# Performance work log

Measured on AMD Instinct MI355X. Metric: run time of the kernel, lower is better.

Reference implementation:

```python
import jax, jax.numpy as jnp
import numpy as np

DIM = 128      # channels C
HEADS = 4
HD = DIM // HEADS  # head_dim = 32
N = 128        # window tokens = 2*8*8
BW = 2048      # B_ = batch * num_windows
NP = 256       # sp_mask partitions
NW = 256       # shift-mask windows
TABLE = 675    # (2*2-1)*(2*8-1)*(2*8-1)
SCALE = HD ** -0.5


def setup_inputs() -> dict:
    key = jax.random.key(0)
    ks = jax.random.split(key, 8)
    x = jax.random.normal(ks[0], (BW, N, DIM), jnp.float32)
    rpi = jax.random.randint(ks[1], (N, N), 0, TABLE, dtype=jnp.int32)
    mask = jax.random.normal(ks[2], (NW, N, N), jnp.float32)
    sp_mask = jax.random.normal(ks[3], (NP, N, N), jnp.float32)
    w_qkv = jax.random.normal(ks[4], (3 * DIM, DIM), jnp.float32) * 0.02
    b_qkv = jnp.zeros((3 * DIM,), jnp.float32)
    bias_table = jax.random.normal(ks[5], (TABLE, HEADS), jnp.float32) * 0.02
    w_proj = jax.random.normal(ks[6], (DIM, DIM), jnp.float32) * 0.02
    b_proj = jnp.zeros((DIM,), jnp.float32)
    return {"x": x, "rpi": rpi, "mask": mask, "sp_mask": sp_mask,
            "w_qkv": w_qkv, "b_qkv": b_qkv, "bias_table": bias_table,
            "w_proj": w_proj, "b_proj": b_proj}


def reference(x, rpi, mask, sp_mask, w_qkv, b_qkv, bias_table, w_proj, b_proj):
    B_, Nn, C = x.shape
    # qkv projection -> (B_, N, 3, H, hd)
    qkv = (x @ w_qkv.T + b_qkv).reshape(B_, Nn, 3, HEADS, HD)
    q = qkv[:, :, 0].transpose(0, 2, 1, 3) * SCALE  # (B_, H, N, hd)
    k = qkv[:, :, 1].transpose(0, 2, 1, 3)
    v = qkv[:, :, 2].transpose(0, 2, 1, 3)
    attn = jnp.einsum('bhnd,bhmd->bhnm', q, k)  # (B_, H, N, N)
    # gathered relative position bias: (N, N, H) -> (H, N, N)
    rpb = bias_table[rpi].transpose(2, 0, 1)
    attn = attn + rpb[None]
    # additive sparse mask, broadcast over B_//nP groups and heads
    attn = (attn.reshape(B_ // NP, NP, HEADS, Nn, Nn)
            + sp_mask[None, :, None]).reshape(B_, HEADS, Nn, Nn)
    # additive shift mask, broadcast over B_//nW groups and heads
    attn = (attn.reshape(B_ // NW, NW, HEADS, Nn, Nn)
            + mask[None, :, None]).reshape(B_, HEADS, Nn, Nn)
    attn = jax.nn.softmax(attn, axis=-1)
    out = jnp.einsum('bhnm,bhmd->bnhd', attn, v).reshape(B_, Nn, C)
    return out @ w_proj.T + b_proj
```

## Files before the change

### kernel.cpp

```cpp
#include <hip/hip_runtime.h>

typedef short v8s __attribute__((ext_vector_type(8)));
typedef float v4f __attribute__((ext_vector_type(4)));

#define MFMA16(a, b, c) __builtin_amdgcn_mfma_f32_16x16x32_bf16(a, b, c, 0, 0, 0)

__device__ __forceinline__ unsigned short f2b(float f) {
  union { float f; unsigned int i; } v;
  v.f = f;
  unsigned int x = v.i;
  return (unsigned short)((x + 0x7fffu + ((x >> 16) & 1u)) >> 16);
}
__device__ __forceinline__ unsigned int cvtpk(float lo, float hi) {
  unsigned int r;
  asm("v_cvt_pk_bf16_f32 %0, %1, %2" : "=v"(r) : "v"(lo), "v"(hi));
  return r;
}

#define SCALE 0.17677669529663687f
#define LOG2E 1.4426950408889634f
#define QSCALE (SCALE * LOG2E)

#define WS_RPB 16777216
#define WS_WQH 17039360
#define WS_WPH 17137664

__global__ __launch_bounds__(256)
void conv_w(const float* __restrict__ wq, const float* __restrict__ wp,
            unsigned short* __restrict__ wqh, unsigned short* __restrict__ wph) {
  int i = blockIdx.x * 256 + threadIdx.x;
  if (i < 384 * 128) wqh[i] = f2b(wq[i]);
  else wph[i - 384 * 128] = f2b(wp[i - 384 * 128]);
}

__global__ __launch_bounds__(256)
void build_bias(const float* __restrict__ mask, const float* __restrict__ sp,
                const int* __restrict__ rpi, const float* __restrict__ btab,
                float* __restrict__ msum, float* __restrict__ rpb) {
  const int wgrp = blockIdx.x, tid = threadIdx.x;
  const float* mk = mask + (size_t)wgrp * 16384;
  const float* sk = sp + (size_t)wgrp * 16384;
  float* ot = msum + (size_t)wgrp * 16384;
  for (int it = 0; it < 16; ++it) {
    int i = (tid + 256 * it) * 4;
    float4 a = *(const float4*)(mk + i);
    float4 b = *(const float4*)(sk + i);
    float4 s;
    s.x = (a.x + b.x) * LOG2E; s.y = (a.y + b.y) * LOG2E;
    s.z = (a.z + b.z) * LOG2E; s.w = (a.w + b.w) * LOG2E;
    *(float4*)(ot + i) = s;
  }
  int e = wgrp * 256 + tid;
  int hh = e >> 14, r = e & 16383;
  rpb[e] = btab[rpi[r] * 4 + hh] * LOG2E;
}

__global__ __launch_bounds__(1024, 4)
void attn_fused(const float* __restrict__ xg,
                const unsigned short* __restrict__ wqh,
                const float* __restrict__ bq,
                const float* __restrict__ msum,
                const float* __restrict__ rpb,
                const unsigned short* __restrict__ wph,
                const float* __restrict__ bpj,
                float* __restrict__ out) {
  __shared__ alignas(16) unsigned char smem[110592];
  unsigned short* xs = (unsigned short*)smem;
  unsigned short* os = (unsigned short*)smem;

  const int tid = threadIdx.x;
  const int wid = tid >> 6;
  const int s = wid & 3;
  const int h = wid >> 2;
  const int lane = tid & 63;
  const int qd = lane >> 4;
  const int t16 = lane & 15;

  const int idx = blockIdx.x;
  const int wgrp = idx >> 3;
  const int b = (idx & 7) * 256 + wgrp;

  unsigned short* kss = (unsigned short*)(smem + 34816 + h * 10240);
  unsigned short* vs  = (unsigned short*)(smem + 75776 + h * 8704);

  {
    const float* src = xg + (size_t)b * 16384;
    for (int it = 0; it < 2; ++it) {
      int gl = tid + 1024 * it;
      int row = gl >> 4, g = gl & 15;
      const float4* s4 = (const float4*)(src + row * 128 + g * 8);
      float4 a = s4[0], c = s4[1];
      union { int4 v; unsigned int d[4]; } pk;
      pk.d[0] = cvtpk(a.x, a.y); pk.d[1] = cvtpk(a.z, a.w);
      pk.d[2] = cvtpk(c.x, c.y); pk.d[3] = cvtpk(c.z, c.w);
      *(int4*)(xs + row * 128 + ((g ^ (row & 15)) << 3)) = pk.v;
    }
  }
  __syncthreads();

  v8s bx[2][4];
  for (int nt = 0; nt < 2; ++nt)
    for (int ks = 0; ks < 4; ++ks) {
      int n = 32 * s + nt * 16 + t16;
      int g = ks * 4 + qd;
      bx[nt][ks] = *(const v8s*)(xs + n * 128 + ((g ^ (n & 15)) << 3));
    }

  v4f accqk[4][2];
  for (int jt = 0; jt < 4; ++jt)
    for (int nt = 0; nt < 2; ++nt) accqk[jt][nt] = v4f{0.f, 0.f, 0.f, 0.f};
  for (int jt = 0; jt < 4; ++jt) {
    int wbase = (jt < 2) ? (h * 32 + jt * 16) : (128 + h * 32 + (jt - 2) * 16);
    for (int ks = 0; ks < 4; ++ks) {
      v8s a = *(const v8s*)(wqh + (wbase + t16) * 128 + ks * 32 + 8 * qd);
      for (int nt = 0; nt < 2; ++nt)
        accqk[jt][nt] = MFMA16(a, bx[nt][ks], accqk[jt][nt]);
    }
  }
  v4f accv[2][2];
  for (int rt = 0; rt < 2; ++rt)
    for (int ct = 0; ct < 2; ++ct) accv[rt][ct] = v4f{0.f, 0.f, 0.f, 0.f};
  for (int ct = 0; ct < 2; ++ct)
    for (int ks = 0; ks < 4; ++ks) {
      v8s bw = *(const v8s*)(wqh + (256 + h * 32 + ct * 16 + t16) * 128 + ks * 32 + 8 * qd);
      for (int rt = 0; rt < 2; ++rt)
        accv[rt][ct] = MFMA16(bx[rt][ks], bw, accv[rt][ct]);
    }

  for (int jt = 2; jt < 4; ++jt)
    for (int nt = 0; nt < 2; ++nt) {
      int n = 32 * s + nt * 16 + t16;
      int bb = 128 + h * 32 + (jt - 2) * 16 + 4 * qd;
      uint2 pk;
      pk.x = cvtpk(accqk[jt][nt][0] + bq[bb + 0], accqk[jt][nt][1] + bq[bb + 1]);
      pk.y = cvtpk(accqk[jt][nt][2] + bq[bb + 2], accqk[jt][nt][3] + bq[bb + 3]);
      *(uint2*)(kss + n * 40 + (jt - 2) * 16 + 4 * qd) = pk;
    }
  for (int ct = 0; ct < 2; ++ct) {
    int d = ct * 16 + t16;
    float bv = bq[256 + h * 32 + d];
    for (int rt = 0; rt < 2; ++rt) {
      uint2 pk;
      pk.x = cvtpk(accv[rt][ct][0] + bv, accv[rt][ct][1] + bv);
      pk.y = cvtpk(accv[rt][ct][2] + bv, accv[rt][ct][3] + bv);
      *(uint2*)(vs + d * 136 + 32 * s + rt * 16 + 4 * qd) = pk;
    }
  }

  unsigned int qpk[2][2][2];
  for (int jt = 0; jt < 2; ++jt)
    for (int nt = 0; nt < 2; ++nt) {
      int bb = h * 32 + jt * 16 + 4 * qd;
      float v0 = (accqk[jt][nt][0] + bq[bb + 0]) * QSCALE;
      float v1 = (accqk[jt][nt][1] + bq[bb + 1]) * QSCALE;
      float v2 = (accqk[jt][nt][2] + bq[bb + 2]) * QSCALE;
      float v3 = (accqk[jt][nt][3] + bq[bb + 3]) * QSCALE;
      qpk[jt][nt][0] = cvtpk(v0, v1);
      qpk[jt][nt][1] = cvtpk(v2, v3);
    }
  const int srcA = ((qd & 1) << 5) + t16;
  const bool hiq = qd >= 2;
  v8s aq[2];
  for (int rt = 0; rt < 2; ++rt) {
    union { v8s v; unsigned int d[4]; } u;
    unsigned int a0 = __shfl((int)qpk[0][rt][0], srcA, 64);
    unsigned int b0 = __shfl((int)qpk[1][rt][0], srcA, 64);
    unsigned int a1 = __shfl((int)qpk[0][rt][1], srcA, 64);
    unsigned int b1 = __shfl((int)qpk[1][rt][1], srcA, 64);
    unsigned int a2 = __shfl((int)qpk[0][rt][0], srcA + 16, 64);
    unsigned int b2 = __shfl((int)qpk[1][rt][0], srcA + 16, 64);
    unsigned int a3 = __shfl((int)qpk[0][rt][1], srcA + 16, 64);
    unsigned int b3 = __shfl((int)qpk[1][rt][1], srcA + 16, 64);
    u.d[0] = hiq ? b0 : a0;
    u.d[1] = hiq ? b1 : a1;
    u.d[2] = hiq ? b2 : a2;
    u.d[3] = hiq ? b3 : a3;
    aq[rt] = u.v;
  }
  __syncthreads();

  v4f sa[2][8];
  const v4f zero4 = {0.f, 0.f, 0.f, 0.f};
  for (int ct = 0; ct < 8; ++ct) {
    v8s bk = *(const v8s*)(kss + (ct * 16 + t16) * 40 + 8 * qd);
    for (int nt = 0; nt < 2; ++nt)
      sa[nt][ct] = MFMA16(bk, aq[nt], zero4);
  }
  {
    const float* mt = msum + (size_t)wgrp * 16384;
    const float* rb = rpb + (size_t)h * 16384;
    for (int nt = 0; nt < 2; ++nt) {
      int n = 32 * s + nt * 16 + t16;
      const float* pm = mt + n * 128;
      const float* pr = rb + n * 128;
      for (int ct = 0; ct < 8; ++ct) {
        float4 b1 = *(const float4*)(pm + ct * 16 + 4 * qd);
        float4 b2 = *(const float4*)(pr + ct * 16 + 4 * qd);
        sa[nt][ct][0] += b1.x + b2.x;
        sa[nt][ct][1] += b1.y + b2.y;
        sa[nt][ct][2] += b1.z + b2.z;
        sa[nt][ct][3] += b1.w + b2.w;
      }
    }
  }
  float pinv[2];
  for (int nt = 0; nt < 2; ++nt) {
    float m0 = sa[nt][0][0];
    for (int ct = 0; ct < 8; ++ct)
      for (int r = 0; r < 4; ++r) m0 = fmaxf(m0, sa[nt][ct][r]);
    m0 = fmaxf(m0, __shfl_xor(m0, 16));
    m0 = fmaxf(m0, __shfl_xor(m0, 32));
    for (int ct = 0; ct < 8; ++ct)
      for (int r = 0; r < 4; ++r)
        sa[nt][ct][r] = exp2f(sa[nt][ct][r] - m0);
    float s0 = 0.f;
    for (int ct = 0; ct < 8; ++ct)
      for (int r = 0; r < 4; ++r) s0 += sa[nt][ct][r];
    s0 += __shfl_xor(s0, 16);
    s0 += __shfl_xor(s0, 32);
    pinv[nt] = 1.0f / s0;
  }

  v8s av[2][4];
  for (int rt = 0; rt < 2; ++rt)
    for (int ks = 0; ks < 4; ++ks)
      av[rt][ks] = *(const v8s*)(vs + (rt * 16 + t16) * 136 + ks * 32 + 8 * qd);

  const int srcP0 = ((qd & 1) << 5) + t16;
  const bool hip2 = qd >= 2;
  for (int nt = 0; nt < 2; ++nt) {
    unsigned int pkd[8][2];
    for (int ct = 0; ct < 8; ++ct) {
      pkd[ct][0] = cvtpk(sa[nt][ct][0], sa[nt][ct][1]);
      pkd[ct][1] = cvtpk(sa[nt][ct][2], sa[nt][ct][3]);
    }
    v8s bp[4];
    for (int ks = 0; ks < 4; ++ks) {
      union { v8s v; unsigned int d[4]; } u;
      unsigned int a0 = __shfl((int)pkd[2 * ks][0], srcP0, 64);
      unsigned int b0 = __shfl((int)pkd[2 * ks + 1][0], srcP0, 64);
      unsigned int a1 = __shfl((int)pkd[2 * ks][1], srcP0, 64);
      unsigned int b1 = __shfl((int)pkd[2 * ks + 1][1], srcP0, 64);
      unsigned int a2 = __shfl((int)pkd[2 * ks][0], srcP0 + 16, 64);
      unsigned int b2 = __shfl((int)pkd[2 * ks + 1][0], srcP0 + 16, 64);
      unsigned int a3 = __shfl((int)pkd[2 * ks][1], srcP0 + 16, 64);
      unsigned int b3 = __shfl((int)pkd[2 * ks + 1][1], srcP0 + 16, 64);
      u.d[0] = hip2 ? b0 : a0;
      u.d[1] = hip2 ? b1 : a1;
      u.d[2] = hip2 ? b2 : a2;
      u.d[3] = hip2 ? b3 : a3;
      bp[ks] = u.v;
    }
    v4f oa[2] = {zero4, zero4};
    for (int ks = 0; ks < 4; ++ks)
      for (int rt = 0; rt < 2; ++rt)
        oa[rt] = MFMA16(av[rt][ks], bp[ks], oa[rt]);
    int n = 32 * s + nt * 16 + t16;
    float sv = pinv[nt];
    for (int rt = 0; rt < 2; ++rt) {
      uint2 pk;
      pk.x = cvtpk(oa[rt][0] * sv, oa[rt][1] * sv);
      pk.y = cvtpk(oa[rt][2] * sv, oa[rt][3] * sv);
      *(uint2*)(os + n * 136 + h * 32 + rt * 16 + 4 * qd) = pk;
    }
  }
  __syncthreads();

  {
    const int tn = wid >> 1;
    const int tc0 = (wid & 1) * 4;
    v8s ao[4];
    for (int ks = 0; ks < 4; ++ks)
      ao[ks] = *(const v8s*)(os + (tn * 16 + t16) * 136 + ks * 32 + 8 * qd);
    for (int tc = 0; tc < 4; ++tc) {
      int co = (tc0 + tc) * 16;
      v4f acc = zero4;
      for (int ks = 0; ks < 4; ++ks) {
        v8s bwp = *(const v8s*)(wph + (co + t16) * 128 + ks * 32 + 8 * qd);
        acc = MFMA16(ao[ks], bwp, acc);
      }
      float bj = bpj[co + t16];
      size_t rowb = (size_t)b * 128 + tn * 16 + 4 * qd;
      out[(rowb + 0) * 128 + co + t16] = acc[0] + bj;
      out[(rowb + 1) * 128 + co + t16] = acc[1] + bj;
      out[(rowb + 2) * 128 + co + t16] = acc[2] + bj;
      out[(rowb + 3) * 128 + co + t16] = acc[3] + bj;
    }
  }
}

extern "C" void kernel_launch(void* const* d_in, const int* in_sizes, int n_in,
                              void* d_out, int out_size, void* d_ws, size_t ws_size,
                              hipStream_t stream) {
  (void)in_sizes; (void)n_in; (void)out_size; (void)ws_size;
  const float* xg   = (const float*)d_in[0];
  const int*   rpi  = (const int*)d_in[1];
  const float* mask = (const float*)d_in[2];
  const float* sp   = (const float*)d_in[3];
  const float* wq   = (const float*)d_in[4];
  const float* bq   = (const float*)d_in[5];
  const float* btab = (const float*)d_in[6];
  const float* wp   = (const float*)d_in[7];
  const float* bpj  = (const float*)d_in[8];
  float* out = (float*)d_out;

  float* msum = (float*)d_ws;
  float* rpb  = (float*)((char*)d_ws + WS_RPB);
  unsigned short* wqh = (unsigned short*)((char*)d_ws + WS_WQH);
  unsigned short* wph = (unsigned short*)((char*)d_ws + WS_WPH);

  conv_w<<<256, 256, 0, stream>>>(wq, wp, wqh, wph);
  build_bias<<<256, 256, 0, stream>>>(mask, sp, rpi, btab, msum, rpb);
  attn_fused<<<2048, 1024, 0, stream>>>(xg, wqh, bq, msum, rpb, wph, bpj, out);
}
```

Baseline: 542.8 us.

## Load x directly into registers, vectorize output stores, widen bias-build grid

Each wave now reads its x fragments straight from global memory and converts them to bf16 in registers. This drops the shared-memory staging pass and the barrier that followed it. The output projection swaps MFMA operands so every lane holds four consecutive output channels, which lets it write float4 stores instead of scattered scalar stores. The bias-build kernel is split across 8x more blocks for more parallelism. In exchange, x is reloaded redundantly across the head waves, which adds global/L2 traffic.

```diff
diff --git a/kernel.cpp b/kernel.cpp
--- a/kernel.cpp
+++ b/kernel.cpp
@@ -15,6 +15,14 @@
   unsigned int r;
   asm("v_cvt_pk_bf16_f32 %0, %1, %2" : "=v"(r) : "v"(lo), "v"(hi));
   return r;
+}
+__device__ __forceinline__ v8s ldf8(const float* p) {
+  float4 a = *(const float4*)p;
+  float4 b = *(const float4*)(p + 4);
+  union { v8s v; unsigned int d[4]; } r;
+  r.d[0] = cvtpk(a.x, a.y); r.d[1] = cvtpk(a.z, a.w);
+  r.d[2] = cvtpk(b.x, b.y); r.d[3] = cvtpk(b.z, b.w);
+  return r.v;
 }
 
 #define SCALE 0.17677669529663687f
@@ -37,11 +45,12 @@
 void build_bias(const float* __restrict__ mask, const float* __restrict__ sp,
                 const int* __restrict__ rpi, const float* __restrict__ btab,
                 float* __restrict__ msum, float* __restrict__ rpb) {
-  const int wgrp = blockIdx.x, tid = threadIdx.x;
-  const float* mk = mask + (size_t)wgrp * 16384;
-  const float* sk = sp + (size_t)wgrp * 16384;
-  float* ot = msum + (size_t)wgrp * 16384;
-  for (int it = 0; it < 16; ++it) {
+  const int wgrp = blockIdx.x >> 3, slab = blockIdx.x & 7, tid = threadIdx.x;
+  const size_t base = (size_t)wgrp * 16384 + slab * 2048;
+  const float* mk = mask + base;
+  const float* sk = sp + base;
+  float* ot = msum + base;
+  for (int it = 0; it < 2; ++it) {
     int i = (tid + 256 * it) * 4;
     float4 a = *(const float4*)(mk + i);
     float4 b = *(const float4*)(sk + i);
@@ -50,9 +59,11 @@
     s.z = (a.z + b.z) * LOG2E; s.w = (a.w + b.w) * LOG2E;
     *(float4*)(ot + i) = s;
   }
-  int e = wgrp * 256 + tid;
-  int hh = e >> 14, r = e & 16383;
-  rpb[e] = btab[rpi[r] * 4 + hh] * LOG2E;
+  int e = blockIdx.x * 256 + tid;
+  if (e < 65536) {
+    int hh = e >> 14, r = e & 16383;
+    rpb[e] = btab[rpi[r] * 4 + hh] * LOG2E;
+  }
 }
 
 __global__ __launch_bounds__(1024, 4)
@@ -65,7 +76,6 @@
                 const float* __restrict__ bpj,
                 float* __restrict__ out) {
   __shared__ alignas(16) unsigned char smem[110592];
-  unsigned short* xs = (unsigned short*)smem;
   unsigned short* os = (unsigned short*)smem;
 
   const int tid = threadIdx.x;
@@ -83,27 +93,12 @@
   unsigned short* kss = (unsigned short*)(smem + 34816 + h * 10240);
   unsigned short* vs  = (unsigned short*)(smem + 75776 + h * 8704);
 
-  {
-    const float* src = xg + (size_t)b * 16384;
-    for (int it = 0; it < 2; ++it) {
-      int gl = tid + 1024 * it;
-      int row = gl >> 4, g = gl & 15;
-      const float4* s4 = (const float4*)(src + row * 128 + g * 8);
-      float4 a = s4[0], c = s4[1];
-      union { int4 v; unsigned int d[4]; } pk;
-      pk.d[0] = cvtpk(a.x, a.y); pk.d[1] = cvtpk(a.z, a.w);
-      pk.d[2] = cvtpk(c.x, c.y); pk.d[3] = cvtpk(c.z, c.w);
-      *(int4*)(xs + row * 128 + ((g ^ (row & 15)) << 3)) = pk.v;
-    }
-  }
-  __syncthreads();
-
+  const float* xb = xg + (size_t)b * 16384;
   v8s bx[2][4];
   for (int nt = 0; nt < 2; ++nt)
     for (int ks = 0; ks < 4; ++ks) {
       int n = 32 * s + nt * 16 + t16;
-      int g = ks * 4 + qd;
-      bx[nt][ks] = *(const v8s*)(xs + n * 128 + ((g ^ (n & 15)) << 3));
+      bx[nt][ks] = ldf8(xb + n * 128 + ks * 32 + 8 * qd);
     }
 
   v4f accqk[4][2];
@@ -268,23 +263,25 @@
 
   {
     const int tn = wid >> 1;
-    const int tc0 = (wid & 1) * 4;
+    const int rh = wid & 1;
     v8s ao[4];
     for (int ks = 0; ks < 4; ++ks)
       ao[ks] = *(const v8s*)(os + (tn * 16 + t16) * 136 + ks * 32 + 8 * qd);
-    for (int tc = 0; tc < 4; ++tc) {
-      int co = (tc0 + tc) * 16;
+    const size_t rowb = ((size_t)b * 128 + tn * 16 + t16) * 128;
+    for (int rt0 = 0; rt0 < 4; ++rt0) {
+      int rt = rh * 4 + rt0;
       v4f acc = zero4;
       for (int ks = 0; ks < 4; ++ks) {
-        v8s bwp = *(const v8s*)(wph + (co + t16) * 128 + ks * 32 + 8 * qd);
-        acc = MFMA16(ao[ks], bwp, acc);
+        v8s a = *(const v8s*)(wph + (rt * 16 + t16) * 128 + ks * 32 + 8 * qd);
+        acc = MFMA16(a, ao[ks], acc);
       }
-      float bj = bpj[co + t16];
-      size_t rowb = (size_t)b * 128 + tn * 16 + 4 * qd;
-      out[(rowb + 0) * 128 + co + t16] = acc[0] + bj;
-      out[(rowb + 1) * 128 + co + t16] = acc[1] + bj;
-      out[(rowb + 2) * 128 + co + t16] = acc[2] + bj;
-      out[(rowb + 3) * 128 + co + t16] = acc[3] + bj;
+      float4 bj = *(const float4*)(bpj + rt * 16 + 4 * qd);
+      float4 pk;
+      pk.x = acc[0] + bj.x;
+      pk.y = acc[1] + bj.y;
+      pk.z = acc[2] + bj.z;
+      pk.w = acc[3] + bj.w;
+      *(float4*)(out + rowb + rt * 16 + 4 * qd) = pk;
     }
   }
 }
@@ -310,6 +307,6 @@
   unsigned short* wph = (unsigned short*)((char*)d_ws + WS_WPH);
 
   conv_w<<<256, 256, 0, stream>>>(wq, wp, wqh, wph);
-  build_bias<<<256, 256, 0, stream>>>(mask, sp, rpi, btab, msum, rpb);
+  build_bias<<<2048, 256, 0, stream>>>(mask, sp, rpi, btab, msum, rpb);
   attn_fused<<<2048, 1024, 0, stream>>>(xg, wqh, bq, msum, rpb, wph, bpj, out);
 }
```

Result: slower. 585.6 us (+7.9%).
